# Kernel optimization log

Hardware: AMD Instinct MI355X
Metric: run time of the kernel (lower is better)

The kernel has to match this reference:

```python
import jax, jax.numpy as jnp
import numpy as np

THR = 1.0      # spiking threshold for encoder and hidden LIF neurons
ALPHA = 0.9    # hidden membrane leak
BETA = 0.9     # output (leaky-integrator) membrane leak
SUR_K = 10.0   # surrogate-gradient sharpness (fwd unaffected)


def _spike(v):
    # Hard Heaviside in fwd, sigmoid surrogate in bwd (straight-through)
    sur = jax.nn.sigmoid(SUR_K * (v - THR))
    hard = (v >= THR).astype(v.dtype)
    return sur + jax.lax.stop_gradient(hard - sur)


def setup_inputs() -> dict:
    key = jax.random.key(0)
    k1, k2, k3 = jax.random.split(key, 3)
    B, T, ORDER, H, C = 512, 1024, 128, 1024, 10
    x = jax.random.normal(k1, (B, T, ORDER), dtype=jnp.float32)
    W_hdn = jax.random.normal(k2, (2 * ORDER, H), dtype=jnp.float32) * (1.0 / np.sqrt(2 * ORDER))
    W_otp = jax.random.normal(k3, (H, C), dtype=jnp.float32) * (1.0 / np.sqrt(H))
    return {"x": x, "W_hdn": W_hdn, "W_otp": W_otp}


def reference(x, W_hdn, W_otp):
    # x: (B, T, ORDER). States are reset (zeros) at the start of each forward,
    # mirroring reset_v()/reset_states() in the torch module.
    B, T, ORDER = x.shape
    H = W_hdn.shape[1]
    C = W_otp.shape[1]
    dt = x.dtype

    xt = jnp.transpose(x, (1, 0, 2))  # (T, B, ORDER) for scan

    def step(carry, x_t):
        v_e, v_h, v_o = carry
        # EncoderLayer: on/off rectified channels -> IF neuron with soft reset
        cur = jnp.concatenate([jax.nn.relu(x_t), jax.nn.relu(-x_t)], axis=-1)  # (B, 2*ORDER)
        v_e = v_e + cur
        s_e = _spike(v_e)
        v_e = v_e - s_e * THR
        # HiddenLayer: LIF with leak ALPHA, soft reset
        v_h = ALPHA * v_h + s_e @ W_hdn
        s_h = _spike(v_h)
        v_h = v_h - s_h * THR
        # OutputLayer: non-spiking leaky integrator; emit membrane potential
        v_o = BETA * v_o + s_h @ W_otp
        return (v_e, v_h, v_o), v_o

    init = (
        jnp.zeros((B, 2 * ORDER), dtype=dt),
        jnp.zeros((B, H), dtype=dt),
        jnp.zeros((B, C), dtype=dt),
    )
    _, m_pots = jax.lax.scan(step, init, xt)  # (T, B, C)
    return jnp.transpose(m_pots, (1, 0, 2))   # (B, T, C) == all_m_pots
```

## Files before the change

### kernel.cpp

```cpp
#include <hip/hip_runtime.h>
#include <hip/hip_bf16.h>


#define BB 512
#define TT 1024
#define OO 128
#define KK 256
#define HH 1024
#define CC 10
#define TC 64
#define NCHUNK (TT / TC)

typedef unsigned long long u64;
typedef __attribute__((ext_vector_type(8))) short short8;
typedef __attribute__((ext_vector_type(4))) float floatx4;
typedef __attribute__((ext_vector_type(4))) int intx4;

__device__ __forceinline__ unsigned short f2bf_rn(float f) {
    unsigned u = __float_as_uint(f);
    u += 0x7FFFu + ((u >> 16) & 1u);
    return (unsigned short)(u >> 16);
}
__device__ __forceinline__ float bf2f(unsigned short h) {
    return __uint_as_float(((unsigned)h) << 16);
}

__device__ __forceinline__ short8 bitsx8_bf16(unsigned e) {
    union { short8 s; unsigned u[4]; } r;
#pragma unroll
    for (int j = 0; j < 4; ++j) {
        unsigned t = (e >> (2 * j)) & 3u;
        r.u[j] = (((t << 15) | t) & 0x10001u) * 0x3F80u;
    }
    return r.s;
}

__device__ __forceinline__ void stage_kt(char* dstbuf ,
                                         const unsigned short* gsrc ,
                                         int kt) {
#pragma unroll
    for (int i = 0; i < 4; ++i) {
        const unsigned short* g = gsrc + (size_t)i * 8 * 512 + kt * 64;
        char* l = dstbuf + i * 1024;
        __builtin_amdgcn_global_load_lds(
            (const __attribute__((address_space(1))) unsigned int*)g,
            (__attribute__((address_space(3))) unsigned int*)l, 16, 0, 0);
    }
}

__global__ __launch_bounds__(128) void k_enc(const float* __restrict__ x,
                                             u64* __restrict__ me) {
    const int b    = blockIdx.x;
    const int j    = threadIdx.x;
    const int wv   = j >> 6;
    const int lane = j & 63;
    const float* xb = x + (size_t)b * (TT * OO);
    float vp = 0.f, vn = 0.f;
    for (int t0 = 0; t0 < TT; t0 += 16) {
        float xs[16];
#pragma unroll
        for (int g = 0; g < 16; ++g) xs[g] = xb[(t0 + g) * OO + j];
#pragma unroll
        for (int g = 0; g < 16; ++g) {
            float xv = xs[g];
            float cp = fmaxf(xv, 0.f);
            float cn = fmaxf(-xv, 0.f);
            vp += cp;
            vn += cn;
            bool sp = (vp >= 1.0f);
            bool sn = (vn >= 1.0f);
            u64 mp = __ballot(sp);
            u64 mn = __ballot(sn);
            if (sp) vp -= 1.0f;
            if (sn) vn -= 1.0f;
            if (lane == 0) {
                size_t r = ((size_t)b * TT + (t0 + g)) * 4;
                me[r + wv]     = mp;
                me[r + 2 + wv] = mn;
            }
        }
    }
}

__global__ __launch_bounds__(256) void k_quant(const float* __restrict__ Wh,
                                               unsigned short* __restrict__ Wt) {
    int idx = blockIdx.x * 256 + threadIdx.x;
    int n = idx >> 9;
    int k = idx & 511;
    float w = Wh[(size_t)(k & 255) * HH + n];
    unsigned short hi = f2bf_rn(w);
    unsigned short out = (k < KK) ? hi : f2bf_rn(w - bf2f(hi));
    Wt[(size_t)n * 512 + k] = out;
}

__global__ __launch_bounds__(256) void k_quant_o(const float* __restrict__ Wo,
                                                 unsigned short* __restrict__ Wqo) {
    int idx = blockIdx.x * 256 + threadIdx.x;
    int n = idx >> 11;
    int k = idx & 2047;
    unsigned short out = 0;
    if (n < CC) {
        float w = Wo[(size_t)(k & 1023) * CC + n];
        unsigned short hi = f2bf_rn(w);
        out = (k < HH) ? hi : f2bf_rn(w - bf2f(hi));
    }
    Wqo[(size_t)n * 2048 + k] = out;
}

__global__ __launch_bounds__(256, 2) void k_gemm_scan(
    const u64* __restrict__ me, const unsigned short* __restrict__ Wt,
    u64* __restrict__ mh) {
    __shared__ __align__(16) char smem[73728];
    char* bufA = smem;
    char* bufB = smem + 16384;
    u64*  Mld  = (u64*)(smem + 65536);

    const int tid  = threadIdx.x;
    const int wave = tid >> 6;
    const int lane = tid & 63;
    const int quad = lane >> 4;
    const int l15  = lane & 15;
    const int mtile = blockIdx.x;
    const int ny    = blockIdx.y;

    const int b = mtile * 4 + wave;
    float vh[2] = {0.f, 0.f};

    const unsigned short* gsrc =
        Wt + (size_t)(ny * 128 + wave * 32 + (lane >> 3)) * 512 +
        (((lane & 7) ^ (lane >> 3)) * 8);
    char* dstA = bufA + wave * 4096;
    char* dstB = bufB + wave * 4096;
    float* scrw = (float*)(smem + wave * 16384);

    for (int ct = 0; ct < NCHUNK; ++ct) {
        const int t0 = ct * TC;

        __syncthreads();
        stage_kt(dstA, gsrc, 0);
        {
            int m  = mtile * 256 + tid;
            int bb = m >> 6;
            int tl = m & 63;
            size_t base = ((size_t)bb * TT + (t0 + tl)) * 4;
#pragma unroll
            for (int w = 0; w < 4; ++w) Mld[w * 256 + tid] = me[base + w];
        }
        __syncthreads();

        floatx4 acc[4][8];
#pragma unroll
        for (int i = 0; i < 4; ++i)
#pragma unroll
            for (int j2 = 0; j2 < 8; ++j2) acc[i][j2] = floatx4{0.f, 0.f, 0.f, 0.f};

#pragma unroll 2
        for (int kt = 0; kt < 8; ++kt) {
            char* rd = (kt & 1) ? bufB : bufA;
            if (kt < 7) stage_kt((kt & 1) ? dstA : dstB, gsrc, kt + 1);

            u64 aw[4];
#pragma unroll
            for (int mg = 0; mg < 4; ++mg)
                aw[mg] = Mld[(kt & 3) * 256 + wave * 64 + mg * 16 + l15];
#pragma unroll
            for (int kw = 0; kw < 2; ++kw) {
                int shift = kw * 32 + quad * 8;
                short8 afrag[4];
#pragma unroll
                for (int mg = 0; mg < 4; ++mg) {
                    unsigned byte = (unsigned)((aw[mg] >> shift) & 0xFFu);
                    afrag[mg] = bitsx8_bf16(byte);
                }
#pragma unroll
                for (int ng = 0; ng < 8; ++ng) {
                    int brow = ng * 16 + l15;
                    int jj = kw * 4 + quad;
                    short8 bfrag = *((const short8*)(rd + brow * 128 + ((jj ^ (brow & 7)) * 16)));
#pragma unroll
                    for (int mg = 0; mg < 4; ++mg)
                        acc[mg][ng] = __builtin_amdgcn_mfma_f32_16x16x32_bf16(
                            afrag[mg], bfrag, acc[mg][ng], 0, 0, 0);
                }
            }
            __syncthreads();
        }

#pragma unroll
        for (int h = 0; h < 2; ++h) {
#pragma unroll
            for (int mg = 0; mg < 4; ++mg)
#pragma unroll
                for (int ng2 = 0; ng2 < 4; ++ng2) {
                    int nl = ng2 * 16 + l15;
                    int p  = mg * 4 + quad;
                    *((floatx4*)((char*)scrw + nl * 256 + ((p ^ l15) * 16))) =
                        acc[mg][h * 4 + ng2];
                }
            float v = vh[h];
            u64 mym = 0;
#pragma unroll
            for (int g = 0; g < 4; ++g) {
                floatx4 cr[4];
#pragma unroll
                for (int q4 = 0; q4 < 4; ++q4) {
                    int p = g * 4 + q4;
                    cr[q4] = *((const floatx4*)((const char*)scrw + lane * 256 +
                                                ((p ^ (lane & 15)) * 16)));
                }
#pragma unroll
                for (int q4 = 0; q4 < 4; ++q4)
#pragma unroll
                    for (int r = 0; r < 4; ++r) {
                        int tl = g * 16 + q4 * 4 + r;
                        v = 0.9f * v + cr[q4][r];
                        bool s = (v >= 1.0f);
                        u64 wm = __ballot(s);
                        if (s) v -= 1.0f;
                        if (lane == tl) mym = wm;
                    }
            }
            mh[((size_t)b * TT + (t0 + lane)) * 16 + ny * 2 + h] = mym;
            vh[h] = v;
        }
    }
}

__global__ __launch_bounds__(256, 2) void k_outcur_mfma(
    const u64* __restrict__ mh, const unsigned short* __restrict__ Wqo,
    float* __restrict__ I) {
    __shared__ __align__(16) char smem[65536];
    char* Bo = smem;

    const int tid  = threadIdx.x;
    const int wave = tid >> 6;
    const int lane = tid & 63;
    const int quad = lane >> 4;
    const int l15  = lane & 15;

    {
#pragma unroll
        for (int i = 0; i < 16; ++i) {
            int pid = i * 256 + tid;
            int n = pid >> 8, p = pid & 255;
            intx4 v = ((const intx4*)Wqo)[pid];
            *((intx4*)(Bo + n * 4096 + ((p ^ (n & 7)) * 16))) = v;
        }
    }
    __syncthreads();

    const int tbase = blockIdx.x * 16 + wave * 4;
    floatx4 acc[4];
#pragma unroll
    for (int tt = 0; tt < 4; ++tt) acc[tt] = floatx4{0.f, 0.f, 0.f, 0.f};

    const u64* rowp[4];
#pragma unroll
    for (int tt = 0; tt < 4; ++tt)
        rowp[tt] = mh + ((size_t)(tbase + tt) * 16 + l15) * 16;

    for (int wi = 0; wi < 16; ++wi) {
        u64 w[4];
#pragma unroll
        for (int tt = 0; tt < 4; ++tt) w[tt] = rowp[tt][wi];
#pragma unroll
        for (int half = 0; half < 2; ++half) {
            int shift = half * 32 + quad * 8;
            int kt_hi = 2 * wi + half;
            int kt_lo = 32 + kt_hi;
            int j_hi = kt_hi * 4 + quad;
            int j_lo = kt_lo * 4 + quad;
            short8 bhi = *((const short8*)(Bo + l15 * 4096 + ((j_hi ^ (l15 & 7)) * 16)));
            short8 blo = *((const short8*)(Bo + l15 * 4096 + ((j_lo ^ (l15 & 7)) * 16)));
#pragma unroll
            for (int tt = 0; tt < 4; ++tt) {
                unsigned byte = (unsigned)((w[tt] >> shift) & 0xFFu);
                short8 af = bitsx8_bf16(byte);
                acc[tt] = __builtin_amdgcn_mfma_f32_16x16x32_bf16(af, bhi, acc[tt], 0, 0, 0);
                acc[tt] = __builtin_amdgcn_mfma_f32_16x16x32_bf16(af, blo, acc[tt], 0, 0, 0);
            }
        }
    }

#pragma unroll
    for (int tt = 0; tt < 4; ++tt)
#pragma unroll
        for (int r = 0; r < 4; ++r) {
            int m = (tbase + tt) * 16 + quad * 4 + r;
            if (l15 < CC) I[(size_t)m * CC + l15] = acc[tt][r];
        }
}

__global__ __launch_bounds__(192) void k_integ1(const float* __restrict__ I,
                                                float* __restrict__ out,
                                                float* __restrict__ vend) {
    int b = blockIdx.x;
    int tid = threadIdx.x;
    if (tid >= 160) return;
    int chunk = tid / 10, c = tid % 10;
    int t0 = chunk * 64;
    const float* Ib = I + ((size_t)b * TT + t0) * CC + c;
    float* ob = out + ((size_t)b * TT + t0) * CC + c;
    float v = 0.f;
    for (int g0 = 0; g0 < 64; g0 += 8) {
        float xs[8];
#pragma unroll
        for (int g = 0; g < 8; ++g) xs[g] = Ib[(g0 + g) * CC];
#pragma unroll
        for (int g = 0; g < 8; ++g) {
            v = 0.9f * v + xs[g];
            ob[(g0 + g) * CC] = v;
        }
    }
    vend[((size_t)b * 16 + chunk) * CC + c] = v;
}

__global__ __launch_bounds__(256) void k_integ2(const float* __restrict__ vend,
                                                float* __restrict__ carry) {
    int id = blockIdx.x * 256 + threadIdx.x;
    if (id >= BB * CC) return;
    int b = id / CC, c = id % CC;
    float d64 = 1.f;
#pragma unroll
    for (int i = 0; i < 64; ++i) d64 *= 0.9f;
    float cv = 0.f;
    for (int k = 0; k < 16; ++k) {
        carry[((size_t)b * 16 + k) * CC + c] = cv;
        cv = vend[((size_t)b * 16 + k) * CC + c] + d64 * cv;
    }
}

__global__ __launch_bounds__(256) void k_integ3(const float* __restrict__ carry,
                                                float* __restrict__ out) {
    __shared__ float dec[64];
    if (threadIdx.x == 0) {
        float d = 1.f;
        for (int i = 0; i < 64; ++i) { d *= 0.9f; dec[i] = d; }
    }
    __syncthreads();
    size_t id = (size_t)blockIdx.x * 256 + threadIdx.x;
    int c = (int)(id % CC);
    size_t bt = id / CC;
    int t = (int)(bt % TT);
    int b = (int)(bt / TT);
    int chunk = t >> 6, tl = t & 63;
    out[id] += dec[tl] * carry[((size_t)b * 16 + chunk) * CC + c];
}

extern "C" void kernel_launch(void* const* d_in, const int* in_sizes, int n_in,
                              void* d_out, int out_size, void* d_ws, size_t ws_size,
                              hipStream_t stream) {
    const float* x  = (const float*)d_in[0];
    const float* Wh = (const float*)d_in[1];
    const float* Wo = (const float*)d_in[2];

    char* p = (char*)d_ws;
    u64* me = (u64*)p;                        p += (size_t)BB * TT * 4 * 8;
    u64* mh = (u64*)p;                        p += (size_t)BB * TT * 16 * 8;
    unsigned short* Wt = (unsigned short*)p;  p += (size_t)HH * 512 * 2;
    float* I = (float*)p;                     p += (size_t)BB * TT * CC * 4;
    unsigned short* Wqo = (unsigned short*)p; p += (size_t)16 * 2048 * 2;
    float* vend  = (float*)Wt;
    float* carry = (float*)(Wt + 512 * 512);

    hipLaunchKernelGGL(k_enc, dim3(BB), dim3(128), 0, stream, x, me);
    hipLaunchKernelGGL(k_quant, dim3(2048), dim3(256), 0, stream, Wh, Wt);
    hipLaunchKernelGGL(k_quant_o, dim3(128), dim3(256), 0, stream, Wo, Wqo);
    hipLaunchKernelGGL(k_gemm_scan, dim3(128, 8), dim3(256), 0, stream, me, Wt, mh);
    hipLaunchKernelGGL(k_outcur_mfma, dim3(2048), dim3(256), 0, stream, mh, Wqo, I);
    hipLaunchKernelGGL(k_integ1, dim3(BB), dim3(192), 0, stream, I, (float*)d_out, vend);
    hipLaunchKernelGGL(k_integ2, dim3(20), dim3(256), 0, stream, vend, carry);
    hipLaunchKernelGGL(k_integ3, dim3(20480), dim3(256), 0, stream, carry, (float*)d_out);
}
```

Measured before the change: 1.056 ms.

## Stage two K-tiles per barrier, precompute LDS offsets, transpose spike mask layout

Restructures the GEMM-scan main loop to stage two K-tiles per step, halving the number of barriers, and precomputes swizzled LDS addresses for the A, B and scratch buffers. It wraps the MFMA bursts in s_setprio to favour the matrix work. It also changes the hidden-spike bitmask output from row-interleaved to a word-major layout, so both the scan stores and the output-current kernel's loads are contiguous across lanes. The shared-memory layout is repacked, with scratch now overlapping the B buffers, which risks subtle aliasing or bank-conflict changes.

```diff
diff --git a/kernel.cpp b/kernel.cpp
--- a/kernel.cpp
+++ b/kernel.cpp
@@ -10,6 +10,7 @@
 #define CC 10
 #define TC 64
 #define NCHUNK (TT / TC)
+#define MTOT ((size_t)BB * TT)
 
 typedef unsigned long long u64;
 typedef __attribute__((ext_vector_type(8))) short short8;
@@ -111,33 +112,45 @@
     const u64* __restrict__ me, const unsigned short* __restrict__ Wt,
     u64* __restrict__ mh) {
     __shared__ __align__(16) char smem[73728];
-    char* bufA = smem;
-    char* bufB = smem + 16384;
-    u64*  Mld  = (u64*)(smem + 65536);
+    u64* Mld = (u64*)smem;
 
     const int tid  = threadIdx.x;
     const int wave = tid >> 6;
     const int lane = tid & 63;
     const int quad = lane >> 4;
     const int l15  = lane & 15;
+    const int h2   = l15 >> 2;
     const int mtile = blockIdx.x;
     const int ny    = blockIdx.y;
 
     const int b = mtile * 4 + wave;
-    float vh[2] = {0.f, 0.f};
+    float vh0 = 0.f, vh1 = 0.f;
 
     const unsigned short* gsrc =
         Wt + (size_t)(ny * 128 + wave * 32 + (lane >> 3)) * 512 +
         (((lane & 7) ^ (lane >> 3)) * 8);
-    char* dstA = bufA + wave * 4096;
-    char* dstB = bufB + wave * 4096;
-    float* scrw = (float*)(smem + wave * 16384);
+    char* dstA = smem + 8192 + wave * 4096;
+    char* dstB = smem + 40960 + wave * 4096;
+
+    const int aoff = wave * 512 + l15 * 8;
+    const int bb0 = 8192 + l15 * 128 + ((quad ^ (l15 & 7)) * 16);
+    const int bb1 = 8192 + l15 * 128 + (((4 + quad) ^ (l15 & 7)) * 16);
+    int sA[4], rA[4];
+    {
+        int sbase = 8192 + wave * 16384 + l15 * 256 + ((quad ^ (l15 & 3)) * 16);
+#pragma unroll
+        for (int mg = 0; mg < 4; ++mg) sA[mg] = sbase + ((mg ^ h2) * 64);
+        int rbase = 8192 + wave * 16384 + lane * 256;
+#pragma unroll
+        for (int q4 = 0; q4 < 4; ++q4) rA[q4] = rbase + ((q4 ^ (l15 & 3)) * 16);
+    }
 
     for (int ct = 0; ct < NCHUNK; ++ct) {
         const int t0 = ct * TC;
 
         __syncthreads();
         stage_kt(dstA, gsrc, 0);
+        stage_kt(dstA + 16384, gsrc, 1);
         {
             int m  = mtile * 256 + tid;
             int bb = m >> 6;
@@ -155,73 +168,75 @@
             for (int j2 = 0; j2 < 8; ++j2) acc[i][j2] = floatx4{0.f, 0.f, 0.f, 0.f};
 
 #pragma unroll 2
-        for (int kt = 0; kt < 8; ++kt) {
-            char* rd = (kt & 1) ? bufB : bufA;
-            if (kt < 7) stage_kt((kt & 1) ? dstA : dstB, gsrc, kt + 1);
-
-            u64 aw[4];
+        for (int rd = 0; rd < 4; ++rd) {
+            if (rd < 3) {
+                char* nxt = (rd & 1) ? dstA : dstB;
+                stage_kt(nxt, gsrc, 2 * rd + 2);
+                stage_kt(nxt + 16384, gsrc, 2 * rd + 3);
+            }
+            const int rofs = (rd & 1) ? 32768 : 0;
+#pragma unroll
+            for (int s = 0; s < 2; ++s) {
+                const int kt = 2 * rd + s;
+                u64 aw[4];
+#pragma unroll
+                for (int mg = 0; mg < 4; ++mg)
+                    aw[mg] = *(const u64*)(smem + aoff +
+                                           ((kt & 3) * 2048 + mg * 128));
+#pragma unroll
+                for (int kw = 0; kw < 2; ++kw) {
+                    const int shift = kw * 32 + quad * 8;
+                    short8 afrag[4];
+#pragma unroll
+                    for (int mg = 0; mg < 4; ++mg)
+                        afrag[mg] = bitsx8_bf16((unsigned)((aw[mg] >> shift) & 0xFFu));
+                    const int bo = kw ? bb1 : bb0;
+                    __builtin_amdgcn_s_setprio(1);
+#pragma unroll
+                    for (int ng = 0; ng < 8; ++ng) {
+                        short8 bfrag = *(const short8*)(
+                            smem + bo + (rofs + s * 16384 + ng * 2048));
+#pragma unroll
+                        for (int mg = 0; mg < 4; ++mg)
+                            acc[mg][ng] = __builtin_amdgcn_mfma_f32_16x16x32_bf16(
+                                afrag[mg], bfrag, acc[mg][ng], 0, 0, 0);
+                    }
+                    __builtin_amdgcn_s_setprio(0);
+                }
+            }
+            __syncthreads();
+        }
+
+#pragma unroll
+        for (int h = 0; h < 2; ++h) {
 #pragma unroll
             for (int mg = 0; mg < 4; ++mg)
-                aw[mg] = Mld[(kt & 3) * 256 + wave * 64 + mg * 16 + l15];
-#pragma unroll
-            for (int kw = 0; kw < 2; ++kw) {
-                int shift = kw * 32 + quad * 8;
-                short8 afrag[4];
-#pragma unroll
-                for (int mg = 0; mg < 4; ++mg) {
-                    unsigned byte = (unsigned)((aw[mg] >> shift) & 0xFFu);
-                    afrag[mg] = bitsx8_bf16(byte);
-                }
-#pragma unroll
-                for (int ng = 0; ng < 8; ++ng) {
-                    int brow = ng * 16 + l15;
-                    int jj = kw * 4 + quad;
-                    short8 bfrag = *((const short8*)(rd + brow * 128 + ((jj ^ (brow & 7)) * 16)));
-#pragma unroll
-                    for (int mg = 0; mg < 4; ++mg)
-                        acc[mg][ng] = __builtin_amdgcn_mfma_f32_16x16x32_bf16(
-                            afrag[mg], bfrag, acc[mg][ng], 0, 0, 0);
-                }
-            }
-            __syncthreads();
-        }
-
-#pragma unroll
-        for (int h = 0; h < 2; ++h) {
-#pragma unroll
-            for (int mg = 0; mg < 4; ++mg)
-#pragma unroll
-                for (int ng2 = 0; ng2 < 4; ++ng2) {
-                    int nl = ng2 * 16 + l15;
-                    int p  = mg * 4 + quad;
-                    *((floatx4*)((char*)scrw + nl * 256 + ((p ^ l15) * 16))) =
-                        acc[mg][h * 4 + ng2];
-                }
-            float v = vh[h];
+#pragma unroll
+                for (int ng2 = 0; ng2 < 4; ++ng2)
+                    *((floatx4*)(smem + sA[mg] + ng2 * 4096)) = acc[mg][h * 4 + ng2];
+            float v = h ? vh1 : vh0;
             u64 mym = 0;
 #pragma unroll
             for (int g = 0; g < 4; ++g) {
+                const int gofs = (g ^ h2) * 64;
                 floatx4 cr[4];
 #pragma unroll
-                for (int q4 = 0; q4 < 4; ++q4) {
-                    int p = g * 4 + q4;
-                    cr[q4] = *((const floatx4*)((const char*)scrw + lane * 256 +
-                                                ((p ^ (lane & 15)) * 16)));
-                }
-#pragma unroll
                 for (int q4 = 0; q4 < 4; ++q4)
+                    cr[q4] = *((const floatx4*)(smem + (rA[q4] + gofs)));
+#pragma unroll
+                for (int q4 = 0; q4 < 4; ++q4)
 #pragma unroll
                     for (int r = 0; r < 4; ++r) {
-                        int tl = g * 16 + q4 * 4 + r;
+                        const int tl = g * 16 + q4 * 4 + r;
                         v = 0.9f * v + cr[q4][r];
-                        bool s = (v >= 1.0f);
-                        u64 wm = __ballot(s);
-                        if (s) v -= 1.0f;
+                        bool sp = (v >= 1.0f);
+                        u64 wm = __ballot(sp);
+                        if (sp) v -= 1.0f;
                         if (lane == tl) mym = wm;
                     }
             }
-            mh[((size_t)b * TT + (t0 + lane)) * 16 + ny * 2 + h] = mym;
-            vh[h] = v;
+            mh[(size_t)(ny * 2 + h) * MTOT + (size_t)b * TT + t0 + lane] = mym;
+            if (h) vh1 = v; else vh0 = v;
         }
     }
 }
@@ -254,15 +269,11 @@
 #pragma unroll
     for (int tt = 0; tt < 4; ++tt) acc[tt] = floatx4{0.f, 0.f, 0.f, 0.f};
 
-    const u64* rowp[4];
-#pragma unroll
-    for (int tt = 0; tt < 4; ++tt)
-        rowp[tt] = mh + ((size_t)(tbase + tt) * 16 + l15) * 16;
-
     for (int wi = 0; wi < 16; ++wi) {
         u64 w[4];
 #pragma unroll
-        for (int tt = 0; tt < 4; ++tt) w[tt] = rowp[tt][wi];
+        for (int tt = 0; tt < 4; ++tt)
+            w[tt] = mh[(size_t)wi * MTOT + (size_t)(tbase + tt) * 16 + l15];
 #pragma unroll
         for (int half = 0; half < 2; ++half) {
             int shift = half * 32 + quad * 8;
```

Result: no change. 1.064 ms (+0.8%).
